# Optimization experiments

Measured on AMD Instinct MI355X. Metric: run time of the kernel, lower is better.

Reference implementation:

```python
import math
import jax, jax.numpy as jnp
import numpy as np

# ---- static config (from init_kwargs) ----
B = 4
FH, FW = 480, 640          # frame size
NSEM = 16
C_OBS = 4 + NSEM           # 20 obs channels (rgb, depth, sem)
C_FEAT = 1 + NSEM          # 17 splatted feature channels
RES = 5.0                  # map resolution cm
VR = 100                   # vision range (cells)
MAXH, MINH = 72, -8        # int(360/5), int(-40/5)
HZ = MAXH - MINH           # 80 height bins
MAP_CELLS = 480            # (4800//2)//5
AGENT_H = 88.0             # camera_height*100
FOV = 79.0
N = FH * FW                # du_scale = 1
MAP_T, EXP_T, CAT_T = 1.0, 1.0, 5.0
DEG = 57.29577951308232
MIN_Z, MAX_Z = 13, 25      # int(25/5 - min_h), int((agent_h+1)/5 - min_h)
X1, X2 = 190, 290          # map crop window
Y1, Y2 = 240, 340


def setup_inputs() -> dict:
    key = jax.random.key(0)
    k1, k2, k3, k4, k5 = jax.random.split(key, 5)
    obs = jax.random.uniform(k1, (B, C_OBS, FH, FW), jnp.float32)
    obs = obs.at[:, 3].multiply(500.0)  # depth channel in cm
    pose_obs = jax.random.normal(k2, (B, 3), jnp.float32) * 0.1
    maps_last = jax.random.uniform(k3, (B, C_OBS, MAP_CELLS, MAP_CELLS), jnp.float32)
    poses_last = jax.random.normal(k4, (B, 3), jnp.float32) * 0.3 \
        + jnp.array([12.0, 12.0, 0.0], jnp.float32)  # near map center (meters, deg)
    sh = jax.random.normal(k5, (B, N, 4), jnp.float32) * 0.1  # SH coeffs per point
    return {"obs": obs, "pose_obs": pose_obs, "maps_last": maps_last,
            "poses_last": poses_last, "sh": sh}


def _affine_grid(theta, H, W):
    # align_corners=True affine grid; theta: (bs, 2, 3) -> (bs, H, W, 2)
    ys = jnp.linspace(-1.0, 1.0, H, dtype=jnp.float32)
    xs = jnp.linspace(-1.0, 1.0, W, dtype=jnp.float32)
    gx, gy = jnp.meshgrid(xs, ys)                       # (H, W)
    base = jnp.stack([gx, gy, jnp.ones_like(gx)], -1)   # (H, W, 3)
    return jnp.einsum('bij,hwj->bhwi', theta, base)


def _grid_sample(img, grid):
    # bilinear, zeros padding, align_corners=True. img: (bs,C,H,W), grid: (bs,H,W,2)
    Bs, C, H, W = img.shape
    x = (grid[..., 0] + 1.0) * (W - 1) / 2.0
    y = (grid[..., 1] + 1.0) * (H - 1) / 2.0
    x0 = jnp.floor(x); y0 = jnp.floor(y)
    x1 = x0 + 1.0; y1 = y0 + 1.0

    def one(img_b, xb, yb, x0b, y0b, x1b, y1b):
        def tap(ix, iy):
            valid = ((ix >= 0) & (ix < W) & (iy >= 0) & (iy < H)).astype(img_b.dtype)
            ic = jnp.clip(ix, 0, W - 1).astype(jnp.int32)
            jc = jnp.clip(iy, 0, H - 1).astype(jnp.int32)
            return img_b[:, jc, ic] * valid[None]        # (C,H,W)
        w00 = (x1b - xb) * (y1b - yb)
        w01 = (xb - x0b) * (y1b - yb)
        w10 = (x1b - xb) * (yb - y0b)
        w11 = (xb - x0b) * (yb - y0b)
        return (tap(x0b, y0b) * w00[None] + tap(x1b, y0b) * w01[None]
                + tap(x0b, y1b) * w10[None] + tap(x1b, y1b) * w11[None])

    return jax.vmap(one)(img, x, y, x0, y0, x1, y1)


def _splat_one(feat_b, coords_b):
    # trilinear scatter-add splat (du.splat_feat_nd). feat_b: (C_FEAT, N), coords_b: (3, N) in [-1,1]
    GD = (VR, VR, HZ)
    grid = jnp.zeros((C_FEAT, VR * VR * HZ), jnp.float32)
    pos = [coords_b[d] * GD[d] / 2.0 + GD[d] / 2.0 for d in range(3)]
    for ix in ((0, 0, 0), (0, 0, 1), (0, 1, 0), (0, 1, 1),
               (1, 0, 0), (1, 0, 1), (1, 1, 0), (1, 1, 1)):
        idx = jnp.zeros((N,), jnp.float32)
        w = jnp.ones((N,), jnp.float32)
        for d in range(3):
            p = jnp.floor(pos[d]) + ix[d]
            safe = ((p > 0) & (p < GD[d])).astype(jnp.float32)
            w = w * (1.0 - jnp.abs(pos[d] - p)) * safe
            idx = idx * GD[d] + p * safe
        grid = grid.at[:, idx.astype(jnp.int32)].add(feat_b * w[None, :])
    return grid


def _forward(obs, pose_obs, maps_last, poses_last, sh):
    bs = obs.shape[0]
    depth = obs[:, 3]                                   # (bs, FH, FW)

    # --- point cloud from depth (du.get_point_cloud_from_z_t) ---
    f = (FW / 2.0) / math.tan(math.radians(FOV / 2.0))
    xc = (FW - 1) / 2.0
    zc = (FH - 1) / 2.0
    gx = jnp.arange(FW, dtype=jnp.float32)
    gz = jnp.arange(FH - 1, -1, -1, dtype=jnp.float32)
    X = (gx[None, None, :] - xc) * depth / f
    Z = (gz[None, :, None] - zc) * depth / f
    # camera view transform (elev=0 -> identity rot, z += agent_h) then
    # shift_loc pose transform (angle pi/2 -> identity rot, x += vr*res//2)
    x_s = X + float(VR * int(RES) // 2)
    y_s = depth
    z_s = Z + AGENT_H

    # --- normalize to [-1,1] voxel coords ---
    xn = (x_s / RES - float(VR // 2)) / VR * 2.0
    yn = (y_s / RES - float(VR // 2)) / VR * 2.0
    zn = (z_s / RES - float((MAXH + MINH) // 2)) / (MAXH - MINH) * 2.0
    coords = jnp.stack([xn, yn, zn], axis=1).reshape(bs, 3, N)
    coords = jnp.clip(coords, -1.0, 1.0)

    # --- features (channel 0 = ones occupancy, rest = semantics; du_scale=1 so avgpool is identity) ---
    feat = jnp.concatenate(
        [jnp.ones((bs, 1, N), jnp.float32), obs[:, 4:].reshape(bs, NSEM, N)], axis=1)
    sh_mean = jnp.mean(sh, axis=2)                      # (bs, N)
    enh = feat * (1.0 + sh_mean[:, None, :])

    # --- voxel splat + round, swap the two xy grid dims (matches .transpose(2,3)) ---
    vox = jax.vmap(_splat_one)(enh, coords)
    vox = jnp.round(vox).reshape(bs, C_FEAT, VR, VR, HZ).transpose(0, 1, 3, 2, 4)

    # --- height projections ---
    agent_proj = vox[..., MIN_Z:MAX_Z].sum(-1)          # (bs, C_FEAT, VR, VR)
    all_proj = vox.sum(-1)
    fp_map_pred = jnp.clip(agent_proj[:, 0:1] / MAP_T, 0.0, 1.0)
    fp_exp_pred = jnp.clip(all_proj[:, 0:1] / EXP_T, 0.0, 1.0)

    # --- write into egocentric map ---
    av = jnp.zeros((bs, C_OBS, MAP_CELLS, MAP_CELLS), jnp.float32)
    av = av.at[:, 0:1, Y1:Y2, X1:X2].set(fp_map_pred)
    av = av.at[:, 1:2, Y1:Y2, X1:X2].set(fp_exp_pred)
    av = av.at[:, 4:, Y1:Y2, X1:X2].set(jnp.clip(agent_proj[:, 1:] / CAT_T, 0.0, 1.0))

    # --- pose integration ---
    t0 = poses_last[:, 2] / DEG
    y_new = poses_last[:, 1] + pose_obs[:, 0] * jnp.sin(t0) + pose_obs[:, 1] * jnp.cos(t0)
    x_new = poses_last[:, 0] + pose_obs[:, 0] * jnp.cos(t0) - pose_obs[:, 1] * jnp.sin(t0)
    t_new = poses_last[:, 2] + pose_obs[:, 2] * DEG
    t_new = jnp.fmod(t_new - 180.0, 360.0) + 180.0
    t_new = jnp.fmod(t_new + 180.0, 360.0) - 180.0
    current_poses = jnp.stack([x_new, y_new, t_new], axis=1)

    # --- spatial transform of egocentric map into allocentric frame ---
    stc = jax.lax.stop_gradient(current_poses)          # matches .clone().detach()
    half = float(MAP_CELLS // 2)                        # 240
    st_xy = -(stc[:, :2] * 100.0 / RES - half) / half
    st_t = (90.0 - stc[:, 2]) * (math.pi / 180.0)
    cos_t, sin_t = jnp.cos(st_t), jnp.sin(st_t)
    zeros = jnp.zeros_like(cos_t); ones = jnp.ones_like(cos_t)
    theta1 = jnp.stack([jnp.stack([cos_t, -sin_t, zeros], 1),
                        jnp.stack([sin_t, cos_t, zeros], 1)], 1)    # (bs,2,3)
    theta2 = jnp.stack([jnp.stack([ones, zeros, st_xy[:, 0]], 1),
                        jnp.stack([zeros, ones, st_xy[:, 1]], 1)], 1)
    rot_grid = _affine_grid(theta1, MAP_CELLS, MAP_CELLS)
    trans_grid = _affine_grid(theta2, MAP_CELLS, MAP_CELLS)
    rotated = _grid_sample(av, rot_grid)
    translated = _grid_sample(rotated, trans_grid)

    map_pred = jnp.maximum(maps_last, translated)
    # pose_pred aliases poses_last which is mutated in-place in torch -> equals current_poses
    return fp_map_pred, map_pred, current_poses, current_poses


def reference(obs, pose_obs, maps_last, poses_last, sh):
    return _forward(obs, pose_obs, maps_last, poses_last, sh)
```

## Files before the change

### kernel.cpp

```cpp
#include <hip/hip_runtime.h>
#include <math.h>

#define FHh 480
#define FWw 640
#define NPIX (FHh*FWw)
#define NSEMC 16
#define COBS 20
#define MAPC 480
#define VRc 100
#define HZc 80
#define MINZc 13
#define MAXZc 25
#define ZW 12
#define NB 4
#define NBINS_DIM 101
#define NBINS_ROW 101
#define NBINS_TOTAL (NB*NBINS_DIM*NBINS_ROW)
#define COUNTS_PAD 40960

__global__ void pose_kernel(const float* __restrict__ pose_obs,
                            const float* __restrict__ poses_last,
                            float* __restrict__ out_p1,
                            float* __restrict__ out_p2,
                            float* __restrict__ params)
{
    int b = threadIdx.x;
    if (b >= NB) return;
    float pl0 = poses_last[b*3+0], pl1 = poses_last[b*3+1], pl2 = poses_last[b*3+2];
    float po0 = pose_obs[b*3+0],  po1 = pose_obs[b*3+1],  po2 = pose_obs[b*3+2];
    const float DEGf = 57.29577951308232f;
    float t0 = pl2 / DEGf;
    float s = sinf(t0), c = cosf(t0);
    float y_new = pl1 + po0*s + po1*c;
    float x_new = pl0 + po0*c - po1*s;
    float t_new = pl2 + po2*DEGf;
    t_new = fmodf(t_new - 180.0f, 360.0f) + 180.0f;
    t_new = fmodf(t_new + 180.0f, 360.0f) - 180.0f;
    out_p1[b*3+0]=x_new; out_p1[b*3+1]=y_new; out_p1[b*3+2]=t_new;
    out_p2[b*3+0]=x_new; out_p2[b*3+1]=y_new; out_p2[b*3+2]=t_new;
    float sx = -(((x_new*100.0f)/5.0f - 240.0f)/240.0f);
    float sy = -(((y_new*100.0f)/5.0f - 240.0f)/240.0f);
    float st_t = (90.0f - t_new) * 0.017453292519943295f;
    params[b*4+0] = cosf(st_t);
    params[b*4+1] = sinf(st_t);
    params[b*4+2] = sx;
    params[b*4+3] = sy;
}

__device__ __forceinline__ float4 pixel_pos(const float* __restrict__ obsb,
                                            const float* __restrict__ sh,
                                            int b, int n, float fconst)
{
    int col = n % FWw, row = n / FWw;
    float depth = obsb[3*NPIX + n];
    const float4 s4 = ((const float4*)sh)[(size_t)b*NPIX + n];
    float sm = (((s4.x + s4.y) + s4.z) + s4.w) / 4.0f;
    float factor = 1.0f + sm;

    float X = ((float)col - 319.5f) * depth / fconst;
    float Z = ((float)(FHh-1-row) - 239.5f) * depth / fconst;
    float x_s = X + 250.0f;
    float z_s = Z + 88.0f;
    float xn = (x_s/5.0f - 50.0f)/100.0f*2.0f;
    float yn = (depth/5.0f - 50.0f)/100.0f*2.0f;
    float zn = (z_s/5.0f - 32.0f)/80.0f*2.0f;
    xn = fminf(fmaxf(xn,-1.0f),1.0f);
    yn = fminf(fmaxf(yn,-1.0f),1.0f);
    zn = fminf(fmaxf(zn,-1.0f),1.0f);
    float pos0 = (xn*100.0f)/2.0f + 50.0f;
    float pos1 = (yn*100.0f)/2.0f + 50.0f;
    float pos2 = (zn*80.0f)/2.0f + 40.0f;
    return make_float4(pos0, pos1, pos2, factor);
}

__global__ void bin_count_kernel(const float* __restrict__ obs,
                                 const float* __restrict__ sh,
                                 float4* __restrict__ tmpPos,
                                 int* __restrict__ auxBid,
                                 int* __restrict__ auxRank,
                                 int* __restrict__ counts,
                                 float fconst)
{
    int g = blockIdx.x*blockDim.x + threadIdx.x;
    if (g >= NB*NPIX) return;
    int b = g / NPIX, n = g % NPIX;
    const float* obsb = obs + (size_t)b*COBS*NPIX;
    float4 P = pixel_pos(obsb, sh, b, n, fconst);
    int f0 = (int)floorf(P.x); if (f0 > 100) f0 = 100;
    int f1 = (int)floorf(P.y); if (f1 > 100) f1 = 100;
    int bid = (b*NBINS_DIM + f0)*NBINS_ROW + f1;
    int r = atomicAdd(&counts[bid], 1);
    tmpPos[g] = P;
    auxBid[g] = bid;
    auxRank[g] = r;
}

__global__ void scan_kernel(int* __restrict__ counts)
{
    __shared__ int part[1024];
    int t = threadIdx.x;
    const int CHUNK = COUNTS_PAD / 1024;
    int base = t*CHUNK;
    int s = 0;
    for (int k = 0; k < CHUNK; ++k) s += counts[base+k];
    part[t] = s;
    __syncthreads();
    for (int off = 1; off < 1024; off <<= 1) {
        int v = (t >= off) ? part[t-off] : 0;
        __syncthreads();
        part[t] += v;
        __syncthreads();
    }
    int run = part[t] - s;
    for (int k = 0; k < CHUNK; ++k) {
        int c = counts[base+k];
        counts[base+k] = run;
        run += c;
    }
}

__global__ void scatter_kernel(const float4* __restrict__ tmpPos,
                               const int* __restrict__ auxBid,
                               const int* __restrict__ auxRank,
                               const int* __restrict__ offsets,
                               float4* __restrict__ payloadPos,
                               int* __restrict__ payloadN)
{
    int g = blockIdx.x*blockDim.x + threadIdx.x;
    if (g >= NB*NPIX) return;
    int dst = offsets[auxBid[g]] + auxRank[g];
    payloadPos[dst] = tmpPos[g];
    payloadN[dst] = g % NPIX;
}

__global__ __launch_bounds__(128)
void gather_kernel(const float* __restrict__ obs,
                   const float4* __restrict__ payloadPos,
                   const int* __restrict__ payloadN,
                   const int* __restrict__ offsets,
                   float* __restrict__ avwin,
                   float* __restrict__ fp_out)
{
    int cell = blockIdx.x;
    int b = blockIdx.y;
    int tid = threadIdx.x;
    int i = cell % VRc, j = cell / VRc;

    __shared__ float acc[HZc + NSEMC*ZW];
    for (int k = tid; k < HZc + NSEMC*ZW; k += 128) acc[k] = 0.0f;
    __syncthreads();

    if (i > 0 && j > 0) {
        const float* obsb = obs + (size_t)b*COBS*NPIX;
        #pragma unroll
        for (int fi = 0; fi < 2; ++fi) {
            int f0r = i - 1 + fi;
            int rb = (b*NBINS_DIM + f0r)*NBINS_ROW;
            int s = offsets[rb + j - 1];
            int e = offsets[rb + j + 1];
            for (int idx = s + tid; idx < e; idx += 128) {
                float4 P = payloadPos[idx];
                float wx = 1.0f - fabsf(P.x - (float)i);
                float wy = 1.0f - fabsf(P.y - (float)j);
                float wxy = wx * wy;
                if (wxy <= 0.0f) continue;
                float f2 = floorf(P.z);
                float wsem0 = 0.0f, wsem1 = 0.0f;
                int qA = (int)f2, qB = qA + 1;
                if (qA > 0 && qA < HZc) {
                    float w = wxy * (1.0f - fabsf(P.z - (float)qA));
                    if (w > 0.0f) {
                        atomicAdd(&acc[qA], P.w * w);
                        if (qA >= MINZc && qA < MAXZc) wsem0 = w;
                    }
                }
                if (qB > 0 && qB < HZc) {
                    float w = wxy * (1.0f - fabsf(P.z - (float)qB));
                    if (w > 0.0f) {
                        atomicAdd(&acc[qB], P.w * w);
                        if (qB >= MINZc && qB < MAXZc) wsem1 = w;
                    }
                }
                if (wsem0 > 0.0f || wsem1 > 0.0f) {
                    int n = payloadN[idx];
                    int zA = qA - MINZc, zB = qB - MINZc;
                    #pragma unroll
                    for (int c = 0; c < NSEMC; ++c) {
                        float enh = obsb[(4+c)*NPIX + n] * P.w;
                        if (wsem0 > 0.0f) atomicAdd(&acc[HZc + c*ZW + zA], enh * wsem0);
                        if (wsem1 > 0.0f) atomicAdd(&acc[HZc + c*ZW + zB], enh * wsem1);
                    }
                }
            }
        }
    }
    __syncthreads();

    float* avb = avwin + (size_t)b*18*10000;
    if (tid < NSEMC) {
        float sum = 0.0f;
        #pragma unroll
        for (int z = 0; z < ZW; ++z) sum += rintf(acc[HZc + tid*ZW + z]);
        avb[(2+tid)*10000 + cell] = fminf(fmaxf(sum/5.0f, 0.0f), 1.0f);
    } else if (tid == 16) {
        float agent = 0.0f;
        #pragma unroll
        for (int z = MINZc; z < MAXZc; ++z) agent += rintf(acc[z]);
        float v = fminf(fmaxf(agent, 0.0f), 1.0f);
        avb[0*10000 + cell] = v;
        fp_out[(size_t)b*10000 + cell] = v;
    } else if (tid == 17) {
        float all = 0.0f;
        for (int z = 0; z < HZc; ++z) all += rintf(acc[z]);
        avb[1*10000 + cell] = fminf(fmaxf(all, 0.0f), 1.0f);
    }
}

__device__ __forceinline__ float grid1d(int i) {
    return (float)(-1.0 + (double)i * (2.0/479.0));
}

__global__ void map_kernel(const float* __restrict__ maps_last,
                           const float* __restrict__ avwin,
                           const float* __restrict__ params,
                           float* __restrict__ map_out)
{
    int t = blockIdx.x*blockDim.x + threadIdx.x;
    if (t >= NB*MAPC*MAPC) return;
    int w = t % MAPC;
    int h = (t / MAPC) % MAPC;
    int b = t / (MAPC*MAPC);
    float ct = params[b*4+0], st = params[b*4+1];
    float sx = params[b*4+2], sy = params[b*4+3];

    float xg = grid1d(w) + sx;
    float yg = grid1d(h) + sy;
    float xt = ((xg + 1.0f)*479.0f)/2.0f;
    float yt = ((yg + 1.0f)*479.0f)/2.0f;
    float xf = floorf(xt), yf = floorf(yt);

    float acc[18];
    #pragma unroll
    for (int k=0;k<18;k++) acc[k]=0.0f;
    const float* avb = avwin + (size_t)b*18*10000;

    #pragma unroll
    for (int oy=0; oy<2; ++oy) {
        #pragma unroll
        for (int ox=0; ox<2; ++ox) {
            float qx = xf + (float)ox, qy = yf + (float)oy;
            if (!(qx >= 0.0f && qx < 480.0f && qy >= 0.0f && qy < 480.0f)) continue;
            float wo = (ox ? (xt - xf) : (xf + 1.0f - xt))
                     * (oy ? (yt - yf) : (yf + 1.0f - yt));
            int oxi = (int)qx, oyi = (int)qy;
            float gxr = grid1d(oxi), gyr = grid1d(oyi);
            float xr = ct*gxr - st*gyr;
            float yr = st*gxr + ct*gyr;
            float xp = ((xr + 1.0f)*479.0f)/2.0f;
            float yp = ((yr + 1.0f)*479.0f)/2.0f;
            float xpf = floorf(xp), ypf = floorf(yp);
            float R[18];
            #pragma unroll
            for (int k=0;k<18;k++) R[k]=0.0f;
            #pragma unroll
            for (int iy=0; iy<2; ++iy) {
                #pragma unroll
                for (int ix=0; ix<2; ++ix) {
                    float rx = xpf + (float)ix, ry = ypf + (float)iy;
                    if (!(rx >= 0.0f && rx < 480.0f && ry >= 0.0f && ry < 480.0f)) continue;
                    int rxi = (int)rx, ryi = (int)ry;
                    if (ryi < 240 || ryi >= 340 || rxi < 190 || rxi >= 290) continue;
                    float wi = (ix ? (xp - xpf) : (xpf + 1.0f - xp))
                             * (iy ? (yp - ypf) : (yp + 1.0f - yp - (yp - ypf)));
                    wi = (ix ? (xp - xpf) : (xpf + 1.0f - xp))
                       * (iy ? (yp - ypf) : (ypf + 1.0f - yp));
                    const float* p = avb + (ryi-240)*VRc + (rxi-190);
                    #pragma unroll
                    for (int k=0;k<18;k++) R[k] += wi * p[k*10000];
                }
            }
            #pragma unroll
            for (int k=0;k<18;k++) acc[k] += wo * R[k];
        }
    }

    #pragma unroll
    for (int c=0;c<COBS;c++) {
        size_t o = (((size_t)b*COBS + c)*MAPC + h)*MAPC + w;
        float tv = (c==0) ? acc[0] : (c==1) ? acc[1] : (c>=4) ? acc[c-2] : 0.0f;
        map_out[o] = fmaxf(maps_last[o], tv);
    }
}

extern "C" void kernel_launch(void* const* d_in, const int* in_sizes, int n_in,
                              void* d_out, int out_size, void* d_ws, size_t ws_size,
                              hipStream_t stream)
{
    const float* obs        = (const float*)d_in[0];
    const float* pose_obs   = (const float*)d_in[1];
    const float* maps_last  = (const float*)d_in[2];
    const float* poses_last = (const float*)d_in[3];
    const float* sh         = (const float*)d_in[4];
    float* out = (float*)d_out;

    float* fp_out  = out;
    float* map_out = out + 40000;
    float* poses1  = out + 40000 + 18432000;
    float* poses2  = poses1 + 12;

    float* params = (float*)d_ws;
    float* avwin  = params + 16;

    const int NTOT = NB*NPIX;
    float4* tmpPos     = (float4*)map_out;
    float4* payloadPos = (float4*)(map_out + 4915200);
    int*    auxBid     = (int*)(map_out + 9830400);
    int*    auxRank    = (int*)(map_out + 11059200);
    int*    payloadN   = (int*)(map_out + 12288000);
    int*    counts     = (int*)(map_out + 13516800);

    double rad = 39.5 * 0.017453292519943295;
    float fconst = (float)(320.0 / tan(rad));

    hipLaunchKernelGGL(pose_kernel, dim3(1), dim3(64), 0, stream,
                       pose_obs, poses_last, poses1, poses2, params);

    hipMemsetAsync(counts, 0, (size_t)COUNTS_PAD*sizeof(int), stream);

    hipLaunchKernelGGL(bin_count_kernel, dim3((NTOT+255)/256), dim3(256), 0, stream,
                       obs, sh, tmpPos, auxBid, auxRank, counts, fconst);

    hipLaunchKernelGGL(scan_kernel, dim3(1), dim3(1024), 0, stream, counts);

    hipLaunchKernelGGL(scatter_kernel, dim3((NTOT+255)/256), dim3(256), 0, stream,
                       tmpPos, auxBid, auxRank, counts, payloadPos, payloadN);

    hipLaunchKernelGGL(gather_kernel, dim3(10000, NB), dim3(128), 0, stream,
                       obs, payloadPos, payloadN, counts, avwin, fp_out);

    hipLaunchKernelGGL(map_kernel, dim3((NB*MAPC*MAPC+255)/256), dim3(256), 0, stream,
                       maps_last, avwin, params, map_out);
}
```

Measured before the change: 812.0 us.

## Restructure point binning: recompute positions, cull non-contributors, pack semantics, tile gather

```diff
diff --git a/kernel.cpp b/kernel.cpp
--- a/kernel.cpp
+++ b/kernel.cpp
@@ -15,8 +15,7 @@
 #define NB 4
 #define NBINS_DIM 101
 #define NBINS_ROW 101
-#define NBINS_TOTAL (NB*NBINS_DIM*NBINS_ROW)
-#define COUNTS_PAD 40960
+#define COUNTS_PAD 20480
 
 __global__ void pose_kernel(const float* __restrict__ pose_obs,
                             const float* __restrict__ poses_last,
@@ -73,29 +72,29 @@
     return make_float4(pos0, pos1, pos2, factor);
 }
 
+__device__ __forceinline__ bool contributes(float4 P) {
+    return (P.x > 0.0f && P.x < 100.0f &&
+            P.y > 0.0f && P.y < 100.0f &&
+            P.z > 0.0f && P.z < 80.0f);
+}
+
 __global__ void bin_count_kernel(const float* __restrict__ obs,
                                  const float* __restrict__ sh,
-                                 float4* __restrict__ tmpPos,
-                                 int* __restrict__ auxBid,
-                                 int* __restrict__ auxRank,
                                  int* __restrict__ counts,
-                                 float fconst)
+                                 float fconst, int bbase)
 {
     int g = blockIdx.x*blockDim.x + threadIdx.x;
-    if (g >= NB*NPIX) return;
-    int b = g / NPIX, n = g % NPIX;
+    if (g >= 2*NPIX) return;
+    int bh = g / NPIX, n = g % NPIX, b = bbase + bh;
     const float* obsb = obs + (size_t)b*COBS*NPIX;
     float4 P = pixel_pos(obsb, sh, b, n, fconst);
-    int f0 = (int)floorf(P.x); if (f0 > 100) f0 = 100;
-    int f1 = (int)floorf(P.y); if (f1 > 100) f1 = 100;
-    int bid = (b*NBINS_DIM + f0)*NBINS_ROW + f1;
-    int r = atomicAdd(&counts[bid], 1);
-    tmpPos[g] = P;
-    auxBid[g] = bid;
-    auxRank[g] = r;
-}
-
-__global__ void scan_kernel(int* __restrict__ counts)
+    if (!contributes(P)) return;
+    int f0 = (int)floorf(P.x);
+    int f1 = (int)floorf(P.y);
+    atomicAdd(&counts[(bh*NBINS_DIM + f0)*NBINS_ROW + f1], 1);
+}
+
+__global__ void scan_kernel(int* __restrict__ counts, int* __restrict__ cursor)
 {
     __shared__ int part[1024];
     int t = threadIdx.x;
@@ -115,80 +114,101 @@
     for (int k = 0; k < CHUNK; ++k) {
         int c = counts[base+k];
         counts[base+k] = run;
+        cursor[base+k] = run;
         run += c;
     }
 }
 
-__global__ void scatter_kernel(const float4* __restrict__ tmpPos,
-                               const int* __restrict__ auxBid,
-                               const int* __restrict__ auxRank,
-                               const int* __restrict__ offsets,
+__global__ void scatter_kernel(const float* __restrict__ obs,
+                               const float* __restrict__ sh,
+                               int* __restrict__ cursor,
                                float4* __restrict__ payloadPos,
-                               int* __restrict__ payloadN)
+                               float* __restrict__ payloadSem,
+                               float fconst, int bbase)
 {
     int g = blockIdx.x*blockDim.x + threadIdx.x;
-    if (g >= NB*NPIX) return;
-    int dst = offsets[auxBid[g]] + auxRank[g];
-    payloadPos[dst] = tmpPos[g];
-    payloadN[dst] = g % NPIX;
-}
-
-__global__ __launch_bounds__(128)
-void gather_kernel(const float* __restrict__ obs,
-                   const float4* __restrict__ payloadPos,
-                   const int* __restrict__ payloadN,
-                   const int* __restrict__ offsets,
+    if (g >= 2*NPIX) return;
+    int bh = g / NPIX, n = g % NPIX, b = bbase + bh;
+    const float* obsb = obs + (size_t)b*COBS*NPIX;
+    float4 P = pixel_pos(obsb, sh, b, n, fconst);
+    if (!contributes(P)) return;
+    int f0 = (int)floorf(P.x);
+    int f1 = (int)floorf(P.y);
+    int bid = (bh*NBINS_DIM + f0)*NBINS_ROW + f1;
+    int dst = atomicAdd(&cursor[bid], 1);
+    payloadPos[dst] = P;
+    int fz = (int)floorf(P.z);
+    if (fz >= MINZc-1 && fz < MAXZc) {
+        float* sp = payloadSem + (size_t)dst*NSEMC;
+        #pragma unroll
+        for (int c = 0; c < NSEMC; ++c)
+            sp[c] = obsb[(4+c)*NPIX + n] * P.w;
+    }
+}
+
+__global__ __launch_bounds__(256)
+void gather_kernel(const float4* __restrict__ payloadPos,
+                   const float* __restrict__ payloadSem,
+                   const int* __restrict__ offs,
                    float* __restrict__ avwin,
-                   float* __restrict__ fp_out)
-{
-    int cell = blockIdx.x;
-    int b = blockIdx.y;
+                   float* __restrict__ fp_out, int bbase)
+{
+    int tile = blockIdx.x;
+    int bh = blockIdx.y, b = bbase + bh;
+    int ti = tile % 50, tj = tile / 50;
+    int i0 = 2*ti, j0 = 2*tj;
     int tid = threadIdx.x;
-    int i = cell % VRc, j = cell / VRc;
-
-    __shared__ float acc[HZc + NSEMC*ZW];
-    for (int k = tid; k < HZc + NSEMC*ZW; k += 128) acc[k] = 0.0f;
+
+    __shared__ float accS[4*272];
+    for (int k = tid; k < 4*272; k += 256) accS[k] = 0.0f;
     __syncthreads();
 
-    if (i > 0 && j > 0) {
-        const float* obsb = obs + (size_t)b*COBS*NPIX;
-        #pragma unroll
-        for (int fi = 0; fi < 2; ++fi) {
-            int f0r = i - 1 + fi;
-            int rb = (b*NBINS_DIM + f0r)*NBINS_ROW;
-            int s = offsets[rb + j - 1];
-            int e = offsets[rb + j + 1];
-            for (int idx = s + tid; idx < e; idx += 128) {
-                float4 P = payloadPos[idx];
-                float wx = 1.0f - fabsf(P.x - (float)i);
-                float wy = 1.0f - fabsf(P.y - (float)j);
-                float wxy = wx * wy;
-                if (wxy <= 0.0f) continue;
-                float f2 = floorf(P.z);
-                float wsem0 = 0.0f, wsem1 = 0.0f;
-                int qA = (int)f2, qB = qA + 1;
-                if (qA > 0 && qA < HZc) {
-                    float w = wxy * (1.0f - fabsf(P.z - (float)qA));
-                    if (w > 0.0f) {
-                        atomicAdd(&acc[qA], P.w * w);
-                        if (qA >= MINZc && qA < MAXZc) wsem0 = w;
-                    }
-                }
-                if (qB > 0 && qB < HZc) {
-                    float w = wxy * (1.0f - fabsf(P.z - (float)qB));
-                    if (w > 0.0f) {
-                        atomicAdd(&acc[qB], P.w * w);
-                        if (qB >= MINZc && qB < MAXZc) wsem1 = w;
-                    }
-                }
-                if (wsem0 > 0.0f || wsem1 > 0.0f) {
-                    int n = payloadN[idx];
-                    int zA = qA - MINZc, zB = qB - MINZc;
+    int f1lo = (j0 > 0) ? (j0-1) : 0;
+    int f1hi = j0 + 1;
+    #pragma unroll
+    for (int t3 = 0; t3 < 3; ++t3) {
+        int f0r = i0 - 1 + t3;
+        if (f0r < 0) continue;
+        int rb = (bh*NBINS_DIM + f0r)*NBINS_ROW;
+        int s = offs[rb + f1lo];
+        int e = offs[rb + f1hi + 1];
+        for (int idx = s + tid; idx < e; idx += 256) {
+            float4 P = payloadPos[idx];
+            int fx = (int)floorf(P.x), fy = (int)floorf(P.y), fz = (int)floorf(P.z);
+            float sem[NSEMC];
+            bool semL = false;
+            #pragma unroll
+            for (int dz = 0; dz < 2; ++dz) {
+                int cz = fz + dz;
+                if (cz <= 0 || cz >= HZc) continue;
+                float wz = 1.0f - fabsf(P.z - (float)cz);
+                if (wz <= 0.0f) continue;
+                bool zwin = (cz >= MINZc && cz < MAXZc);
+                #pragma unroll
+                for (int dy = 0; dy < 2; ++dy) {
+                    int cy = fy + dy, jy = cy - j0;
+                    if ((unsigned)jy > 1u || cy == 0) continue;
+                    float wyz = wz * (1.0f - fabsf(P.y - (float)cy));
                     #pragma unroll
-                    for (int c = 0; c < NSEMC; ++c) {
-                        float enh = obsb[(4+c)*NPIX + n] * P.w;
-                        if (wsem0 > 0.0f) atomicAdd(&acc[HZc + c*ZW + zA], enh * wsem0);
-                        if (wsem1 > 0.0f) atomicAdd(&acc[HZc + c*ZW + zB], enh * wsem1);
+                    for (int dx = 0; dx < 2; ++dx) {
+                        int cx = fx + dx, ix = cx - i0;
+                        if ((unsigned)ix > 1u || cx == 0) continue;
+                        float w = wyz * (1.0f - fabsf(P.x - (float)cx));
+                        if (w <= 0.0f) continue;
+                        int base = (jy*2 + ix)*272;
+                        atomicAdd(&accS[base + cz], P.w * w);
+                        if (zwin) {
+                            if (!semL) {
+                                #pragma unroll
+                                for (int c = 0; c < NSEMC; ++c)
+                                    sem[c] = payloadSem[(size_t)idx*NSEMC + c];
+                                semL = true;
+                            }
+                            int zo = base + HZc + (cz - MINZc);
+                            #pragma unroll
+                            for (int c = 0; c < NSEMC; ++c)
+                                atomicAdd(&accS[zo + c*ZW], sem[c] * w);
+                        }
                     }
                 }
             }
@@ -196,23 +216,30 @@
     }
     __syncthreads();
 
-    float* avb = avwin + (size_t)b*18*10000;
-    if (tid < NSEMC) {
-        float sum = 0.0f;
-        #pragma unroll
-        for (int z = 0; z < ZW; ++z) sum += rintf(acc[HZc + tid*ZW + z]);
-        avb[(2+tid)*10000 + cell] = fminf(fmaxf(sum/5.0f, 0.0f), 1.0f);
-    } else if (tid == 16) {
-        float agent = 0.0f;
-        #pragma unroll
-        for (int z = MINZc; z < MAXZc; ++z) agent += rintf(acc[z]);
-        float v = fminf(fmaxf(agent, 0.0f), 1.0f);
-        avb[0*10000 + cell] = v;
-        fp_out[(size_t)b*10000 + cell] = v;
-    } else if (tid == 17) {
-        float all = 0.0f;
-        for (int z = 0; z < HZc; ++z) all += rintf(acc[z]);
-        avb[1*10000 + cell] = fminf(fmaxf(all, 0.0f), 1.0f);
+    if (tid < 72) {
+        int cellL = tid / 18, ch = tid % 18;
+        int ci = i0 + (cellL & 1), cj = j0 + (cellL >> 1);
+        const float* a = &accS[cellL*272];
+        float* avb = avwin + (size_t)b*18*10000;
+        int oidx = cj*VRc + ci;
+        if (ch == 0) {
+            float s0 = 0.0f;
+            #pragma unroll
+            for (int z = MINZc; z < MAXZc; ++z) s0 += rintf(a[z]);
+            float v = fminf(fmaxf(s0, 0.0f), 1.0f);
+            avb[oidx] = v;
+            fp_out[(size_t)b*10000 + oidx] = v;
+        } else if (ch == 1) {
+            float s0 = 0.0f;
+            for (int z = 0; z < HZc; ++z) s0 += rintf(a[z]);
+            avb[10000 + oidx] = fminf(fmaxf(s0, 0.0f), 1.0f);
+        } else {
+            int c = ch - 2;
+            float s0 = 0.0f;
+            #pragma unroll
+            for (int z = 0; z < ZW; ++z) s0 += rintf(a[HZc + c*ZW + z]);
+            avb[ch*10000 + oidx] = fminf(fmaxf(s0/5.0f, 0.0f), 1.0f);
+        }
     }
 }
 
@@ -271,9 +298,7 @@
                     int rxi = (int)rx, ryi = (int)ry;
                     if (ryi < 240 || ryi >= 340 || rxi < 190 || rxi >= 290) continue;
                     float wi = (ix ? (xp - xpf) : (xpf + 1.0f - xp))
-                             * (iy ? (yp - ypf) : (yp + 1.0f - yp - (yp - ypf)));
-                    wi = (ix ? (xp - xpf) : (xpf + 1.0f - xp))
-                       * (iy ? (yp - ypf) : (ypf + 1.0f - yp));
+                             * (iy ? (yp - ypf) : (ypf + 1.0f - yp));
                     const float* p = avb + (ryi-240)*VRc + (rxi-190);
                     #pragma unroll
                     for (int k=0;k<18;k++) R[k] += wi * p[k*10000];
@@ -311,13 +336,11 @@
     float* params = (float*)d_ws;
     float* avwin  = params + 16;
 
-    const int NTOT = NB*NPIX;
-    float4* tmpPos     = (float4*)map_out;
-    float4* payloadPos = (float4*)(map_out + 4915200);
-    int*    auxBid     = (int*)(map_out + 9830400);
-    int*    auxRank    = (int*)(map_out + 11059200);
-    int*    payloadN   = (int*)(map_out + 12288000);
-    int*    counts     = (int*)(map_out + 13516800);
+    const int NHALF = 2*NPIX;
+    float4* payloadPos = (float4*)map_out;
+    float*  payloadSem = map_out + 2457600;
+    int*    counts     = (int*)(map_out + 12288000);
+    int*    cursor     = (int*)(map_out + 12288000 + 20480);
 
     double rad = 39.5 * 0.017453292519943295;
     float fconst = (float)(320.0 / tan(rad));
@@ -325,18 +348,17 @@
     hipLaunchKernelGGL(pose_kernel, dim3(1), dim3(64), 0, stream,
                        pose_obs, poses_last, poses1, poses2, params);
 
-    hipMemsetAsync(counts, 0, (size_t)COUNTS_PAD*sizeof(int), stream);
-
-    hipLaunchKernelGGL(bin_count_kernel, dim3((NTOT+255)/256), dim3(256), 0, stream,
-                       obs, sh, tmpPos, auxBid, auxRank, counts, fconst);
-
-    hipLaunchKernelGGL(scan_kernel, dim3(1), dim3(1024), 0, stream, counts);
-
-    hipLaunchKernelGGL(scatter_kernel, dim3((NTOT+255)/256), dim3(256), 0, stream,
-                       tmpPos, auxBid, auxRank, counts, payloadPos, payloadN);
-
-    hipLaunchKernelGGL(gather_kernel, dim3(10000, NB), dim3(128), 0, stream,
-                       obs, payloadPos, payloadN, counts, avwin, fp_out);
+    for (int half = 0; half < 2; ++half) {
+        int bbase = 2*half;
+        hipMemsetAsync(counts, 0, (size_t)COUNTS_PAD*sizeof(int), stream);
+        hipLaunchKernelGGL(bin_count_kernel, dim3((NHALF+255)/256), dim3(256), 0, stream,
+                           obs, sh, counts, fconst, bbase);
+        hipLaunchKernelGGL(scan_kernel, dim3(1), dim3(1024), 0, stream, counts, cursor);
+        hipLaunchKernelGGL(scatter_kernel, dim3((NHALF+255)/256), dim3(256), 0, stream,
+                           obs, sh, cursor, payloadPos, payloadSem, fconst, bbase);
+        hipLaunchKernelGGL(gather_kernel, dim3(2500, 2), dim3(256), 0, stream,
+                           payloadPos, payloadSem, counts, avwin, fp_out, bbase);
+    }
 
     hipLaunchKernelGGL(map_kernel, dim3((NB*MAPC*MAPC+255)/256), dim3(256), 0, stream,
                        maps_last, avwin, params, map_out);
```

Measured after the change: 1.013 ms. 24.8% more time.
